# Performance work log

Hardware: AMD Instinct MI355X
Metric: run time of the kernel (lower is better)

The kernel has to match this reference:

```python
import jax, jax.numpy as jnp
import numpy as np

N = 200000      # nodes (Elliptic-scale transaction graph)
E = 400000      # directed edges
F_IN = 165      # node features
HID = 128
OUT = 2


def setup_inputs() -> dict:
    key = jax.random.key(0)
    k = jax.random.split(key, 5)
    x = jax.random.normal(k[0], (N, F_IN), dtype=jnp.float32)
    edge_index = jax.random.randint(k[1], (2, E), 0, N, dtype=jnp.int32)
    # GCNConv params (PyG: Linear without bias semantics differ slightly by
    # version; here weight + bias, bias added after aggregation)
    W1 = jax.random.normal(k[2], (F_IN, HID), dtype=jnp.float32) * (1.0 / np.sqrt(F_IN))
    b1 = jnp.zeros((HID,), dtype=jnp.float32)
    W2 = jax.random.normal(k[3], (HID, OUT), dtype=jnp.float32) * (1.0 / np.sqrt(HID))
    b2 = jnp.zeros((OUT,), dtype=jnp.float32)
    return {"x": x, "edge_index": edge_index, "W1": W1, "b1": b1, "W2": W2, "b2": b2}


def _gcn_conv(h, edge_index, W, b):
    """PyG GCNConv: out = D^{-1/2} (A + I) D^{-1/2} (h @ W) + b."""
    h = h @ W                                    # [N, F_out]
    loop = jnp.arange(N, dtype=edge_index.dtype)
    src = jnp.concatenate([edge_index[0], loop])  # add self-loops
    dst = jnp.concatenate([edge_index[1], loop])
    # degree over destination nodes (self-loops guarantee deg >= 1)
    deg = jax.ops.segment_sum(jnp.ones_like(dst, dtype=h.dtype), dst, num_segments=N)
    dinv = jax.lax.rsqrt(deg)
    norm = dinv[src] * dinv[dst]                 # [E+N]
    msgs = h[src] * norm[:, None]                # gather + scale
    out = jax.ops.segment_sum(msgs, dst, num_segments=N)  # scatter-add
    return out + b


def reference(x, edge_index, W1, b1, W2, b2):
    h = _gcn_conv(x, edge_index, W1, b1)
    # torch.relu then F.dropout(training=False) (identity) then torch.relu:
    # in eval mode relu(relu(h)) == relu(h)
    h = jnp.maximum(h, 0.0)
    return _gcn_conv(h, edge_index, W2, b2)
```

## Files before the change

kernel.cpp:

```cpp
#include <hip/hip_runtime.h>
#include <hip/hip_bf16.h>

typedef __attribute__((ext_vector_type(8))) short bf16x8;
typedef __attribute__((ext_vector_type(4))) float f32x4;

#define N_NODES 200000
#define N_EDGES 400000
#define F_IN    165
#define HID     128
#define N_TILES 3125
#define KSTEPS  6
#define CAP     32

__device__ __forceinline__ uint bf16r(float f) {
  uint u = __float_as_uint(f);
  return (u + 0x7FFFu + ((u >> 16) & 1u)) >> 16;
}

__device__ __forceinline__ void gload16(const void* gp, void* lp) {
  __builtin_amdgcn_global_load_lds(
      (const __attribute__((address_space(1))) unsigned int*)gp,
      (__attribute__((address_space(3))) unsigned int*)lp, 16, 0, 0);
}


__global__ __launch_bounds__(256) void k_init(const float* __restrict__ W1,
                                              ushort* __restrict__ Wf,
                                              uint4* __restrict__ cursor) {
  int b = blockIdx.x;
  int tid = threadIdx.x;
  if (b < 96) {
    int id = b * 256 + tid;
    int j = id & 7;
    int lane = (id >> 3) & 63;
    int rem = id >> 9;
    int s = rem % 6;
    int ct = rem / 6;
    int k = s * 32 + (lane >> 4) * 8 + j;
    int col = ct * 16 + (lane & 15);
    float v = (k < F_IN) ? W1[k * HID + col] : 0.f;
    Wf[id] = (ushort)bf16r(v);
  } else {
    int i = (b - 96) * 256 + tid;
    if (i < 50000) cursor[i] = make_uint4(0, 0, 0, 0);
  }
}


__global__ __launch_bounds__(256) void k_place(const int* __restrict__ ei,
                                               int* __restrict__ cursor,
                                               int* __restrict__ slots) {
  int e = blockIdx.x * 256 + threadIdx.x;
  if (e < N_EDGES) {
    int d = ei[N_EDGES + e];
    int pos = atomicAdd(&cursor[d], 1);
    if (pos < CAP) slots[d * CAP + pos] = ei[e];
  }
}


__global__ __launch_bounds__(256) void k_gemm1(const float* __restrict__ x,
                                               const ushort* __restrict__ Wf,
                                               const int* __restrict__ cursor,
                                               uint* __restrict__ g) {
  __shared__ float xs[64 * F_IN];
  const int tid  = threadIdx.x;
  const int wave = tid >> 6;
  const int lane = tid & 63;
  const int r15  = lane & 15;
  const int kg   = lane >> 4;

  bf16x8 bfrag[2][KSTEPS];
  #pragma unroll
  for (int t = 0; t < 2; ++t) {
    int ct = wave * 2 + t;
    #pragma unroll
    for (int s = 0; s < KSTEPS; ++s)
      bfrag[t][s] = *(const bf16x8*)(Wf + (size_t)(((ct * KSTEPS + s) * 64 + lane) << 3));
  }

  const size_t tb = (size_t)blockIdx.x * (64 * F_IN);
  #pragma unroll
  for (int it = 0; it < 10; ++it) {
    gload16(x + tb + (size_t)(it * 256 + tid) * 4,
            (char*)xs + (size_t)(it * 256 + wave * 64) * 16);
  }
  if (tid < 80) {
    int c = 2560 + tid;
    *(float4*)((char*)xs + (size_t)c * 16) = *(const float4*)(x + tb + (size_t)c * 4);
  }
  __syncthreads();

  f32x4 acc[4][2];
  #pragma unroll
  for (int rg = 0; rg < 4; ++rg) {
    acc[rg][0] = (f32x4){0.f, 0.f, 0.f, 0.f};
    acc[rg][1] = (f32x4){0.f, 0.f, 0.f, 0.f};
  }

  #pragma unroll
  for (int rg = 0; rg < 4; ++rg) {
    const float* rp0 = xs + (rg * 16 + r15) * F_IN;
    #pragma unroll
    for (int s = 0; s < KSTEPS; ++s) {
      uint o0, o1, o2, o3;
      if (s < 5) {
        const float* rp = rp0 + s * 32 + kg * 8;
        o0 = bf16r(rp[0]) | (bf16r(rp[1]) << 16);
        o1 = bf16r(rp[2]) | (bf16r(rp[3]) << 16);
        o2 = bf16r(rp[4]) | (bf16r(rp[5]) << 16);
        o3 = bf16r(rp[6]) | (bf16r(rp[7]) << 16);
      } else {
        o0 = o1 = o2 = o3 = 0u;
        if (kg == 0) {
          const float* rp = rp0 + 160;
          o0 = bf16r(rp[0]) | (bf16r(rp[1]) << 16);
          o1 = bf16r(rp[2]) | (bf16r(rp[3]) << 16);
          o2 = bf16r(rp[4]);
        }
      }
      uint4 uu = make_uint4(o0, o1, o2, o3);
      bf16x8 a = *(bf16x8*)&uu;
      acc[rg][0] = __builtin_amdgcn_mfma_f32_16x16x32_bf16(a, bfrag[0][s], acc[rg][0], 0, 0, 0);
      acc[rg][1] = __builtin_amdgcn_mfma_f32_16x16x32_bf16(a, bfrag[1][s], acc[rg][1], 0, 0, 0);
    }
  }

  int base = blockIdx.x * 64;
  #pragma unroll
  for (int rg = 0; rg < 4; ++rg) {
    #pragma unroll
    for (int r = 0; r < 4; ++r) {
      int row = base + rg * 16 + kg * 4 + r;
      float dv = rsqrtf(1.0f + (float)cursor[row]);
      uint u = bf16r(acc[rg][0][r] * dv) | (bf16r(acc[rg][1][r] * dv) << 16);
      g[(size_t)row * 64 + wave * 16 + r15] = u;
    }
  }
}


__global__ __launch_bounds__(256) void k_agg1(const uint* __restrict__ g,
                                              const int* __restrict__ cursor,
                                              const int* __restrict__ slots,
                                              const float* __restrict__ b1,
                                              const float* __restrict__ W2,
                                              float* __restrict__ g2) {
  const int tid  = threadIdx.x;
  const int lane = tid & 63;
  const int wave = tid >> 6;
  const int sub  = lane >> 4;
  const int fl   = lane & 15;

  float  b1lo[4], b1hi[4];
  float2 w2lo[4], w2hi[4];
  #pragma unroll
  for (int k = 0; k < 4; ++k) {
    int dw = fl * 4 + k;
    int c0 = ((dw >> 4) << 5) + (dw & 15);
    b1lo[k] = b1[c0];
    b1hi[k] = b1[c0 + 16];
    w2lo[k] = *(const float2*)&W2[c0 * 2];
    w2hi[k] = *(const float2*)&W2[(c0 + 16) * 2];
  }

  int degs[8], slotv[8];
  #pragma unroll
  for (int it = 0; it < 8; ++it) {
    int node = blockIdx.x * 128 + it * 16 + wave * 4 + sub;
    int cn = min(node, N_NODES - 1);
    degs[it]  = cursor[cn];
    slotv[it] = slots[cn * CAP + fl];
  }

  #pragma unroll
  for (int it = 0; it < 8; ++it) {
    int node = blockIdx.x * 128 + it * 16 + wave * 4 + sub;
    if (node < N_NODES) {
      int deg = degs[it];
      float dv = rsqrtf(1.0f + (float)deg);
      int dcap = min(deg, 16);
      int srcl = (fl < dcap) ? slotv[it] : node;

      uint4 v = *(const uint4*)&g[(size_t)node * 64 + fl * 4];
      float sx0 = __uint_as_float(v.x << 16), sy0 = __uint_as_float(v.x & 0xFFFF0000u);
      float sx1 = __uint_as_float(v.y << 16), sy1 = __uint_as_float(v.y & 0xFFFF0000u);
      float sx2 = __uint_as_float(v.z << 16), sy2 = __uint_as_float(v.z & 0xFFFF0000u);
      float sx3 = __uint_as_float(v.w << 16), sy3 = __uint_as_float(v.w & 0xFFFF0000u);

      #pragma unroll
      for (int j = 0; j < 4; ++j) {
        int s = __shfl(srcl, sub * 16 + j);
        float wj = (j < dcap) ? 1.f : 0.f;
        uint4 w = *(const uint4*)&g[(size_t)s * 64 + fl * 4];
        sx0 = fmaf(__uint_as_float(w.x << 16), wj, sx0);
        sy0 = fmaf(__uint_as_float(w.x & 0xFFFF0000u), wj, sy0);
        sx1 = fmaf(__uint_as_float(w.y << 16), wj, sx1);
        sy1 = fmaf(__uint_as_float(w.y & 0xFFFF0000u), wj, sy1);
        sx2 = fmaf(__uint_as_float(w.z << 16), wj, sx2);
        sy2 = fmaf(__uint_as_float(w.z & 0xFFFF0000u), wj, sy2);
        sx3 = fmaf(__uint_as_float(w.w << 16), wj, sx3);
        sy3 = fmaf(__uint_as_float(w.w & 0xFFFF0000u), wj, sy3);
      }
      for (int j = 4; j < dcap; ++j) {
        int s = __shfl(srcl, sub * 16 + j);
        uint4 w = *(const uint4*)&g[(size_t)s * 64 + fl * 4];
        sx0 += __uint_as_float(w.x << 16); sy0 += __uint_as_float(w.x & 0xFFFF0000u);
        sx1 += __uint_as_float(w.y << 16); sy1 += __uint_as_float(w.y & 0xFFFF0000u);
        sx2 += __uint_as_float(w.z << 16); sy2 += __uint_as_float(w.z & 0xFFFF0000u);
        sx3 += __uint_as_float(w.w << 16); sy3 += __uint_as_float(w.w & 0xFFFF0000u);
      }
      for (int e = 16; e < min(deg, CAP); ++e) {
        uint4 w = *(const uint4*)&g[(size_t)slots[node * CAP + e] * 64 + fl * 4];
        sx0 += __uint_as_float(w.x << 16); sy0 += __uint_as_float(w.x & 0xFFFF0000u);
        sx1 += __uint_as_float(w.y << 16); sy1 += __uint_as_float(w.y & 0xFFFF0000u);
        sx2 += __uint_as_float(w.z << 16); sy2 += __uint_as_float(w.z & 0xFFFF0000u);
        sx3 += __uint_as_float(w.w << 16); sy3 += __uint_as_float(w.w & 0xFFFF0000u);
      }

      float h, p0 = 0.f, p1 = 0.f;
      h = fmaxf(fmaf(sx0, dv, b1lo[0]), 0.f); p0 = fmaf(h, w2lo[0].x, p0); p1 = fmaf(h, w2lo[0].y, p1);
      h = fmaxf(fmaf(sy0, dv, b1hi[0]), 0.f); p0 = fmaf(h, w2hi[0].x, p0); p1 = fmaf(h, w2hi[0].y, p1);
      h = fmaxf(fmaf(sx1, dv, b1lo[1]), 0.f); p0 = fmaf(h, w2lo[1].x, p0); p1 = fmaf(h, w2lo[1].y, p1);
      h = fmaxf(fmaf(sy1, dv, b1hi[1]), 0.f); p0 = fmaf(h, w2hi[1].x, p0); p1 = fmaf(h, w2hi[1].y, p1);
      h = fmaxf(fmaf(sx2, dv, b1lo[2]), 0.f); p0 = fmaf(h, w2lo[2].x, p0); p1 = fmaf(h, w2lo[2].y, p1);
      h = fmaxf(fmaf(sy2, dv, b1hi[2]), 0.f); p0 = fmaf(h, w2hi[2].x, p0); p1 = fmaf(h, w2hi[2].y, p1);
      h = fmaxf(fmaf(sx3, dv, b1lo[3]), 0.f); p0 = fmaf(h, w2lo[3].x, p0); p1 = fmaf(h, w2lo[3].y, p1);
      h = fmaxf(fmaf(sy3, dv, b1hi[3]), 0.f); p0 = fmaf(h, w2hi[3].x, p0); p1 = fmaf(h, w2hi[3].y, p1);

      #pragma unroll
      for (int off = 1; off < 16; off <<= 1) {
        p0 += __shfl_xor(p0, off);
        p1 += __shfl_xor(p1, off);
      }
      if (fl == 0) {
        *(float2*)&g2[(size_t)node * 2] = make_float2(p0 * dv, p1 * dv);
      }
    }
  }
}


__global__ __launch_bounds__(256) void k_agg2(const float2* __restrict__ g2,
                                              const int* __restrict__ cursor,
                                              const int* __restrict__ slots,
                                              const float* __restrict__ b2,
                                              float* __restrict__ out) {
  int i = blockIdx.x * 256 + threadIdx.x;
  if (i >= N_NODES) return;
  float2 s = g2[i];
  int deg = cursor[i];
  int dcap = min(deg, CAP);
  for (int e = 0; e < dcap; ++e) {
    float2 m = g2[slots[i * CAP + e]];
    s.x += m.x;
    s.y += m.y;
  }
  float dv = rsqrtf(1.0f + (float)deg);
  float2 o;
  o.x = fmaf(s.x, dv, b2[0]);
  o.y = fmaf(s.y, dv, b2[1]);
  *(float2*)&out[(size_t)i * 2] = o;
}


extern "C" void kernel_launch(void* const* d_in, const int* in_sizes, int n_in,
                              void* d_out, int out_size, void* d_ws, size_t ws_size,
                              hipStream_t stream) {
  const float* x  = (const float*)d_in[0];
  const int*   ei = (const int*)d_in[1];
  const float* W1 = (const float*)d_in[2];
  const float* b1 = (const float*)d_in[3];
  const float* W2 = (const float*)d_in[4];
  const float* b2 = (const float*)d_in[5];
  float* out = (float*)d_out;

  char* ws = (char*)d_ws;
  size_t off = 0;
  auto take = [&](size_t bytes) -> char* {
    char* p = ws + off;
    off = (off + bytes + 255) & ~(size_t)255;
    return p;
  };
  int*    cursor = (int*)   take((size_t)N_NODES * 4);
  int*    slots  = (int*)   take((size_t)N_NODES * CAP * 4);
  float*  g2     = (float*) take((size_t)N_NODES * 2 * 4);
  ushort* Wf     = (ushort*)take((size_t)8 * KSTEPS * 64 * 8 * 2);
  uint*   g      = (uint*)  take((size_t)N_NODES * 64 * 4);
  (void)ws_size; (void)in_sizes; (void)n_in; (void)out_size;

  k_init<<<292, 256, 0, stream>>>(W1, Wf, (uint4*)cursor);
  k_place<<<1563, 256, 0, stream>>>(ei, cursor, slots);
  k_gemm1<<<N_TILES, 256, 0, stream>>>(x, Wf, cursor, g);
  k_agg1<<<1563, 256, 0, stream>>>(g, cursor, slots, b1, W2, g2);
  k_agg2<<<(N_NODES + 255) / 256, 256, 0, stream>>>((const float2*)g2, cursor,
                                                    slots, b2, out);
}
```

Baseline: 106.6 us.

## Fuse edge bucketing into GEMM kernel and move source-degree scaling into aggregation

The edge placement pass is folded into the first GEMM kernel: each of the 3125 blocks places 128 edges (3125 × 128 = 400000), which removes one kernel launch and lets the atomic bucketing overlap with the x tile loads and MFMA work. Because degrees are no longer final when the GEMM writes its output, the source-side D^-1/2 scaling moves into the aggregation kernel. That kernel now reads cursor[s] for each neighbor and applies rsqrt per edge. The cost is an extra random 4-byte load and an rsqrt per gathered edge, plus atomics competing with the GEMM for memory bandwidth.

After: 102.8 us. 3.5% less time.

```diff
diff --git a/kernel.cpp b/kernel.cpp
--- a/kernel.cpp
+++ b/kernel.cpp
@@ -47,28 +47,25 @@
 }
 
 
-__global__ __launch_bounds__(256) void k_place(const int* __restrict__ ei,
-                                               int* __restrict__ cursor,
-                                               int* __restrict__ slots) {
-  int e = blockIdx.x * 256 + threadIdx.x;
-  if (e < N_EDGES) {
-    int d = ei[N_EDGES + e];
-    int pos = atomicAdd(&cursor[d], 1);
-    if (pos < CAP) slots[d * CAP + pos] = ei[e];
-  }
-}
-
-
-__global__ __launch_bounds__(256) void k_gemm1(const float* __restrict__ x,
-                                               const ushort* __restrict__ Wf,
-                                               const int* __restrict__ cursor,
-                                               uint* __restrict__ g) {
+__global__ __launch_bounds__(256) void k_gemm1p(const float* __restrict__ x,
+                                                const ushort* __restrict__ Wf,
+                                                const int* __restrict__ ei,
+                                                int* __restrict__ cursor,
+                                                int* __restrict__ slots,
+                                                uint* __restrict__ g) {
   __shared__ float xs[64 * F_IN];
   const int tid  = threadIdx.x;
   const int wave = tid >> 6;
   const int lane = tid & 63;
   const int r15  = lane & 15;
   const int kg   = lane >> 4;
+
+  if (tid < 128) {
+    int e = blockIdx.x * 128 + tid;
+    int d = ei[N_EDGES + e];
+    int pos = atomicAdd(&cursor[d], 1);
+    if (pos < CAP) slots[d * CAP + pos] = ei[e];
+  }
 
   bf16x8 bfrag[2][KSTEPS];
   #pragma unroll
@@ -132,8 +129,7 @@
     #pragma unroll
     for (int r = 0; r < 4; ++r) {
       int row = base + rg * 16 + kg * 4 + r;
-      float dv = rsqrtf(1.0f + (float)cursor[row]);
-      uint u = bf16r(acc[rg][0][r] * dv) | (bf16r(acc[rg][1][r] * dv) << 16);
+      uint u = bf16r(acc[rg][0][r]) | (bf16r(acc[rg][1][r]) << 16);
       g[(size_t)row * 64 + wave * 16 + r15] = u;
     }
   }
@@ -183,15 +179,15 @@
       int srcl = (fl < dcap) ? slotv[it] : node;
 
       uint4 v = *(const uint4*)&g[(size_t)node * 64 + fl * 4];
-      float sx0 = __uint_as_float(v.x << 16), sy0 = __uint_as_float(v.x & 0xFFFF0000u);
-      float sx1 = __uint_as_float(v.y << 16), sy1 = __uint_as_float(v.y & 0xFFFF0000u);
-      float sx2 = __uint_as_float(v.z << 16), sy2 = __uint_as_float(v.z & 0xFFFF0000u);
-      float sx3 = __uint_as_float(v.w << 16), sy3 = __uint_as_float(v.w & 0xFFFF0000u);
+      float sx0 = dv * __uint_as_float(v.x << 16), sy0 = dv * __uint_as_float(v.x & 0xFFFF0000u);
+      float sx1 = dv * __uint_as_float(v.y << 16), sy1 = dv * __uint_as_float(v.y & 0xFFFF0000u);
+      float sx2 = dv * __uint_as_float(v.z << 16), sy2 = dv * __uint_as_float(v.z & 0xFFFF0000u);
+      float sx3 = dv * __uint_as_float(v.w << 16), sy3 = dv * __uint_as_float(v.w & 0xFFFF0000u);
 
       #pragma unroll
       for (int j = 0; j < 4; ++j) {
         int s = __shfl(srcl, sub * 16 + j);
-        float wj = (j < dcap) ? 1.f : 0.f;
+        float wj = (j < dcap) ? rsqrtf(1.0f + (float)cursor[s]) : 0.f;
         uint4 w = *(const uint4*)&g[(size_t)s * 64 + fl * 4];
         sx0 = fmaf(__uint_as_float(w.x << 16), wj, sx0);
         sy0 = fmaf(__uint_as_float(w.x & 0xFFFF0000u), wj, sy0);
@@ -204,18 +200,29 @@
       }
       for (int j = 4; j < dcap; ++j) {
         int s = __shfl(srcl, sub * 16 + j);
+        float wj = rsqrtf(1.0f + (float)cursor[s]);
         uint4 w = *(const uint4*)&g[(size_t)s * 64 + fl * 4];
-        sx0 += __uint_as_float(w.x << 16); sy0 += __uint_as_float(w.x & 0xFFFF0000u);
-        sx1 += __uint_as_float(w.y << 16); sy1 += __uint_as_float(w.y & 0xFFFF0000u);
-        sx2 += __uint_as_float(w.z << 16); sy2 += __uint_as_float(w.z & 0xFFFF0000u);
-        sx3 += __uint_as_float(w.w << 16); sy3 += __uint_as_float(w.w & 0xFFFF0000u);
+        sx0 = fmaf(__uint_as_float(w.x << 16), wj, sx0);
+        sy0 = fmaf(__uint_as_float(w.x & 0xFFFF0000u), wj, sy0);
+        sx1 = fmaf(__uint_as_float(w.y << 16), wj, sx1);
+        sy1 = fmaf(__uint_as_float(w.y & 0xFFFF0000u), wj, sy1);
+        sx2 = fmaf(__uint_as_float(w.z << 16), wj, sx2);
+        sy2 = fmaf(__uint_as_float(w.z & 0xFFFF0000u), wj, sy2);
+        sx3 = fmaf(__uint_as_float(w.w << 16), wj, sx3);
+        sy3 = fmaf(__uint_as_float(w.w & 0xFFFF0000u), wj, sy3);
       }
       for (int e = 16; e < min(deg, CAP); ++e) {
-        uint4 w = *(const uint4*)&g[(size_t)slots[node * CAP + e] * 64 + fl * 4];
-        sx0 += __uint_as_float(w.x << 16); sy0 += __uint_as_float(w.x & 0xFFFF0000u);
-        sx1 += __uint_as_float(w.y << 16); sy1 += __uint_as_float(w.y & 0xFFFF0000u);
-        sx2 += __uint_as_float(w.z << 16); sy2 += __uint_as_float(w.z & 0xFFFF0000u);
-        sx3 += __uint_as_float(w.w << 16); sy3 += __uint_as_float(w.w & 0xFFFF0000u);
+        int s = slots[node * CAP + e];
+        float wj = rsqrtf(1.0f + (float)cursor[s]);
+        uint4 w = *(const uint4*)&g[(size_t)s * 64 + fl * 4];
+        sx0 = fmaf(__uint_as_float(w.x << 16), wj, sx0);
+        sy0 = fmaf(__uint_as_float(w.x & 0xFFFF0000u), wj, sy0);
+        sx1 = fmaf(__uint_as_float(w.y << 16), wj, sx1);
+        sy1 = fmaf(__uint_as_float(w.y & 0xFFFF0000u), wj, sy1);
+        sx2 = fmaf(__uint_as_float(w.z << 16), wj, sx2);
+        sy2 = fmaf(__uint_as_float(w.z & 0xFFFF0000u), wj, sy2);
+        sx3 = fmaf(__uint_as_float(w.w << 16), wj, sx3);
+        sy3 = fmaf(__uint_as_float(w.w & 0xFFFF0000u), wj, sy3);
       }
 
       float h, p0 = 0.f, p1 = 0.f;
@@ -290,8 +297,7 @@
   (void)ws_size; (void)in_sizes; (void)n_in; (void)out_size;
 
   k_init<<<292, 256, 0, stream>>>(W1, Wf, (uint4*)cursor);
-  k_place<<<1563, 256, 0, stream>>>(ei, cursor, slots);
-  k_gemm1<<<N_TILES, 256, 0, stream>>>(x, Wf, cursor, g);
+  k_gemm1p<<<N_TILES, 256, 0, stream>>>(x, Wf, ei, cursor, slots, g);
   k_agg1<<<1563, 256, 0, stream>>>(g, cursor, slots, b1, W2, g2);
   k_agg2<<<(N_NODES + 255) / 256, 256, 0, stream>>>((const float2*)g2, cursor,
                                                     slots, b2, out);
```
